# Kernel optimization log

Hardware: AMD Instinct MI355X
Metric: run time of the kernel (lower is better)

## Reference

```python
import jax, jax.numpy as jnp
import numpy as np

M, N, K = 1024, 11008, 4096


def _unpack_i2u(Bp):
    """Unpack 2-bit unsigned weights per decode_i2u_to_i8s interleave.

    Bp: [N, K//4] int8 storage. Within each group of 4 bytes (16 elements),
    output element at position 4*i + j = (byte_j >> (2*i)) & 3.
    Returns [N, K] int8 with values in {0,1,2,3}.
    """
    Bu = jax.lax.bitcast_convert_type(Bp, jnp.uint8)  # [N, K//4]
    n, kc = Bu.shape
    Bg = Bu.reshape(n, kc // 4, 1, 4)                 # [N, G, 1, j]
    shifts = (jnp.arange(4, dtype=jnp.uint8) * jnp.uint8(2)).reshape(1, 1, 4, 1)
    vals = (Bg >> shifts) & jnp.uint8(3)              # [N, G, i, j]
    return vals.reshape(n, kc * 4).astype(jnp.int8)   # [N, K]


def setup_inputs() -> dict:
    key = jax.random.key(0)
    k1, k2 = jax.random.split(key)
    A = jax.random.randint(k1, (M, K), -128, 128, dtype=jnp.int8)
    B = jax.random.randint(k2, (N, K // 4), -128, 128, dtype=jnp.int8)
    return {"A": A, "B": B}


def reference(A, B):
    W = _unpack_i2u(B)  # [N, K] int8
    C = jax.lax.dot_general(
        A, W,
        dimension_numbers=(((1,), (1,)), ((), ())),
        preferred_element_type=jnp.int32,
    )  # [M, N] int32
    return C
```

## Files before the change

### kernel.cpp

```cpp
#include <hip/hip_runtime.h>
#include <stdint.h>


#define MM 1024
#define NN 11008
#define KK 4096
#define MTILES 8
#define NTILES 86
#define NBLOCKS (16 * NTILES)
#define STRIDE_A ((size_t)MTILES * 8192)
#define STRIDE_B ((size_t)NTILES * 2048)

using i32x4  = __attribute__((ext_vector_type(4))) int;
using i32x16 = __attribute__((ext_vector_type(16))) int;

__device__ __forceinline__ int pack4(i32x4 v) {
    return (int)(((uint32_t)v[0] & 0xFFu) | (((uint32_t)v[1] & 0xFFu) << 8)
               | (((uint32_t)v[2] & 0xFFu) << 16) | (((uint32_t)v[3] & 0xFFu) << 24));
}

__global__ __launch_bounds__(256) void prep_AB(const int* __restrict__ Asrc,
                                               const int* __restrict__ Bsrc,
                                               uint8_t* __restrict__ A2,
                                               uint8_t* __restrict__ B3) {
    if (blockIdx.x < 1024) {
        const int g = blockIdx.x * 256 + threadIdx.x;
        const int kstep = g >> 12;
        const int rem   = g & 4095;
        const int mtile = rem >> 9;
        const int c     = rem & 511;
        const int row32 = (c >> 7) & 3, kk2 = (c >> 6) & 1;
        const int lane  = c & 63;
        const int row   = mtile * 128 + row32 * 32 + (lane & 31);
        const int kbyte = kstep * 64 + kk2 * 32 + (lane >> 5) * 16;
        const i32x4* s4 = (const i32x4*)(Asrc + (size_t)row * KK + kbyte);
        i32x4 o;
#pragma unroll
        for (int q = 0; q < 4; ++q) o[q] = pack4(s4[q]);
        *(i32x4*)(A2 + (size_t)g * 16) = o;
    } else {
        const int t = (blockIdx.x - 1024) * 256 + threadIdx.x;
        const int n = t >> 6, kstep = t & 63;
        const int ntile = n >> 7, hf = (n >> 6) & 1, ni = (n >> 5) & 1, l31 = n & 31;
        const i32x4* s4 = (const i32x4*)(Bsrc + (size_t)n * (KK / 4) + kstep * 16);
        int w[4];
#pragma unroll
        for (int j = 0; j < 4; ++j) w[j] = pack4(s4[j]);
        uint8_t* base = B3 + ((size_t)kstep * NTILES + ntile) * 2048 + hf * 1024;
        *(int2*)(base + l31 * 16 + ni * 8)        = make_int2(w[0], w[2]);
        *(int2*)(base + (l31 + 32) * 16 + ni * 8) = make_int2(w[1], w[3]);
    }
}

#define GLOAD_LDS16(g, l) __builtin_amdgcn_global_load_lds(                    \
        (const __attribute__((address_space(1))) uint32_t*)(g),                \
        (__attribute__((address_space(3))) uint32_t*)(l), 16, 0, 0)

#define MFMA_I8 __builtin_amdgcn_mfma_i32_32x32x32_i8

#define STAGE(T) do {                                                          \
    const uint8_t* at_ = gA + (size_t)((T) + 3) * STRIDE_A;                    \
    uint8_t* ls_ = &As[wid][((T) + 3) & 3][0];                                 \
    GLOAD_LDS16(at_,        ls_);                                              \
    GLOAD_LDS16(at_ + 1024, ls_ + 1024);                                       \
    GLOAD_LDS16(at_ + 2048, ls_ + 2048);                                       \
    GLOAD_LDS16(at_ + 3072, ls_ + 3072);                                       \
} while (0)

#define BLOAD(BI, T) do {                                                      \
    c0[BI] = *(const i32x4*)(gB + (size_t)(T) * STRIDE_B);                     \
    c1[BI] = *(const i32x4*)(gB + (size_t)(T) * STRIDE_B + 1024);              \
} while (0)

#define COMP(T, BI) do {                                                       \
    const uint8_t* ab_ = &As[wid][(T) & 3][0];                                 \
    i32x4 a00 = *(const i32x4*)(ab_ + lane * 16);                              \
    i32x4 a01 = *(const i32x4*)(ab_ + 1024 + lane * 16);                       \
    i32x4 a10 = *(const i32x4*)(ab_ + 2048 + lane * 16);                       \
    i32x4 a11 = *(const i32x4*)(ab_ + 3072 + lane * 16);                       \
    _Pragma("unroll")                                                          \
    for (int kk2_ = 0; kk2_ < 2; ++kk2_) {                                     \
        const uint32_t q0_ = (uint32_t)c0[BI][kk2_];                           \
        const uint32_t q1_ = (uint32_t)c0[BI][2 + kk2_];                       \
        const uint32_t q2_ = (uint32_t)c1[BI][kk2_];                           \
        const uint32_t q3_ = (uint32_t)c1[BI][2 + kk2_];                       \
        i32x4 b0_, b1_, b2_, b3_;                                              \
        _Pragma("unroll")                                                      \
        for (int i_ = 0; i_ < 4; ++i_) {                                       \
            b0_[i_] = (int)((q0_ >> (2 * i_)) & 0x03030303u);                  \
            b1_[i_] = (int)((q1_ >> (2 * i_)) & 0x03030303u);                  \
            b2_[i_] = (int)((q2_ >> (2 * i_)) & 0x03030303u);                  \
            b3_[i_] = (int)((q3_ >> (2 * i_)) & 0x03030303u);                  \
        }                                                                      \
        const i32x4 am0_ = kk2_ ? a01 : a00;                                   \
        const i32x4 am1_ = kk2_ ? a11 : a10;                                   \
        __builtin_amdgcn_s_setprio(1);                                         \
        acc[0][0] = MFMA_I8(am0_, b0_, acc[0][0], 0, 0, 0);                    \
        acc[0][1] = MFMA_I8(am0_, b1_, acc[0][1], 0, 0, 0);                    \
        acc[0][2] = MFMA_I8(am0_, b2_, acc[0][2], 0, 0, 0);                    \
        acc[0][3] = MFMA_I8(am0_, b3_, acc[0][3], 0, 0, 0);                    \
        acc[1][0] = MFMA_I8(am1_, b0_, acc[1][0], 0, 0, 0);                    \
        acc[1][1] = MFMA_I8(am1_, b1_, acc[1][1], 0, 0, 0);                    \
        acc[1][2] = MFMA_I8(am1_, b2_, acc[1][2], 0, 0, 0);                    \
        acc[1][3] = MFMA_I8(am1_, b3_, acc[1][3], 0, 0, 0);                    \
        __builtin_amdgcn_s_setprio(0);                                         \
    }                                                                          \
} while (0)

#define ITER(T, BCUR, BNXT, NW, DOSTAGE, DOB) do {                             \
    if (DOSTAGE) STAGE(T);                                                     \
    if (DOB)     BLOAD(BNXT, (T) + 2);                                         \
    asm volatile("s_waitcnt vmcnt(" #NW ")" ::: "memory");                     \
    __builtin_amdgcn_sched_barrier(0);                                         \
    COMP(T, BCUR);                                                             \
} while (0)

__global__ __launch_bounds__(128, 2) void bitnet_gemm(const uint8_t* __restrict__ A2,
                                                      const uint8_t* __restrict__ B3,
                                                      int* __restrict__ C) {
    const int tid  = threadIdx.x;
    const int lane = tid & 63, wid = tid >> 6;
    const int l31  = lane & 31, h = lane >> 5;

    const int bid = blockIdx.x;
    const int l   = (bid & 7) * (NBLOCKS / 8) + (bid >> 3);
    const int wm  = l & 15;
    const int wn  = l >> 4;

    __shared__ __align__(16) uint8_t As[2][4][4096];

    const uint8_t* gA = A2 + (size_t)(wid * 32) * STRIDE_A + wm * 4096 + lane * 16;
    const uint8_t* gB = B3 + (size_t)(wid * 32) * STRIDE_B + (size_t)wn * 2048 + lane * 16;

    i32x16 acc[2][4] = {};
    i32x4 c0[3], c1[3];

    STAGE(-3); STAGE(-2); STAGE(-1);
    BLOAD(0, 0); BLOAD(1, 1);

    ITER(0, 0, 2, 8, 1, 1);
    ITER(1, 1, 0, 8, 1, 1);
#pragma unroll 1
    for (int t = 2; t < 29; t += 3) {
        ITER(t,     2, 1, 12, 1, 1);
        ITER(t + 1, 0, 2, 12, 1, 1);
        ITER(t + 2, 1, 0, 12, 1, 1);
    }
    ITER(29, 2, 1, 8, 0, 1);
    ITER(30, 0, 0, 2, 0, 0);
    ITER(31, 1, 0, 0, 0, 0);

    __syncthreads();
    i32x4* red = (i32x4*)&As[0][0][0];
    if (wid == 1) {
#pragma unroll
        for (int mi = 0; mi < 2; ++mi)
#pragma unroll
            for (int nc = 0; nc < 4; ++nc) {
                const i32x16 v = acc[mi][nc];
#pragma unroll
                for (int q = 0; q < 4; ++q) {
                    i32x4 s;
                    s[0] = v[q * 4 + 0]; s[1] = v[q * 4 + 1];
                    s[2] = v[q * 4 + 2]; s[3] = v[q * 4 + 3];
                    red[((mi * 4 + nc) * 4 + q) * 64 + lane] = s;
                }
            }
    }
    __syncthreads();
    if (wid == 0) {
        const int brow = wm * 64, bcol = wn * 128;
#pragma unroll
        for (int mi = 0; mi < 2; ++mi)
#pragma unroll
            for (int nc = 0; nc < 4; ++nc) {
                i32x16 v = acc[mi][nc];
#pragma unroll
                for (int q = 0; q < 4; ++q) {
                    const i32x4 r = red[((mi * 4 + nc) * 4 + q) * 64 + lane];
                    v[q * 4 + 0] += r[0]; v[q * 4 + 1] += r[1];
                    v[q * 4 + 2] += r[2]; v[q * 4 + 3] += r[3];
                }
                const int colg = bcol + nc * 32 + l31;
#pragma unroll
                for (int r = 0; r < 16; ++r) {
                    const int rowin = (r & 3) + 8 * (r >> 2) + 4 * h;
                    const int rowg  = brow + mi * 32 + rowin;
                    C[(size_t)rowg * NN + colg] = v[r];
                }
            }
    }
}

extern "C" void kernel_launch(void* const* d_in, const int* in_sizes, int n_in,
                              void* d_out, int out_size, void* d_ws, size_t ws_size,
                              hipStream_t stream) {
    const int* A32 = (const int*)d_in[0];
    const int* B32 = (const int*)d_in[1];
    int* C = (int*)d_out;

    uint8_t* A2 = (uint8_t*)d_ws;
    uint8_t* B3 = A2 + (size_t)MM * KK;

    prep_AB<<<dim3(1024 + 2752), dim3(256), 0, stream>>>(A32, B32, A2, B3);
    bitnet_gemm<<<dim3(NBLOCKS), dim3(128), 0, stream>>>(A2, B3, C);
}
```

Baseline: 78.32 us.

## Split the N tile across waves instead of split-K, dropping the LDS reduction

The two waves in a block used to split K and each hold the full 64x128 accumulator tile, which forced a reduction through LDS at the end. Now each wave covers a 64x64 half of the N tile over the whole K range, so accumulators halve and the reduction and its barriers disappear. With the smaller register footprint, the launch bounds rise to 3 blocks per EU. The cost is that both waves now stage the same A tile into separate LDS buffers, doubling A load traffic. The pipeline also runs twice as many K iterations, each with half the MFMA work.

```diff
diff --git a/kernel.cpp b/kernel.cpp
--- a/kernel.cpp
+++ b/kernel.cpp
@@ -67,10 +67,7 @@
     GLOAD_LDS16(at_ + 3072, ls_ + 3072);                                       \
 } while (0)
 
-#define BLOAD(BI, T) do {                                                      \
-    c0[BI] = *(const i32x4*)(gB + (size_t)(T) * STRIDE_B);                     \
-    c1[BI] = *(const i32x4*)(gB + (size_t)(T) * STRIDE_B + 1024);              \
-} while (0)
+#define BLOAD(BI, T) bbuf[BI] = *(const i32x4*)(gB + (size_t)(T) * STRIDE_B)
 
 #define COMP(T, BI) do {                                                       \
     const uint8_t* ab_ = &As[wid][(T) & 3][0];                                 \
@@ -80,29 +77,21 @@
     i32x4 a11 = *(const i32x4*)(ab_ + 3072 + lane * 16);                       \
     _Pragma("unroll")                                                          \
     for (int kk2_ = 0; kk2_ < 2; ++kk2_) {                                     \
-        const uint32_t q0_ = (uint32_t)c0[BI][kk2_];                           \
-        const uint32_t q1_ = (uint32_t)c0[BI][2 + kk2_];                       \
-        const uint32_t q2_ = (uint32_t)c1[BI][kk2_];                           \
-        const uint32_t q3_ = (uint32_t)c1[BI][2 + kk2_];                       \
-        i32x4 b0_, b1_, b2_, b3_;                                              \
+        const uint32_t q0_ = (uint32_t)bbuf[BI][kk2_];                         \
+        const uint32_t q1_ = (uint32_t)bbuf[BI][2 + kk2_];                     \
+        i32x4 b0_, b1_;                                                        \
         _Pragma("unroll")                                                      \
         for (int i_ = 0; i_ < 4; ++i_) {                                       \
             b0_[i_] = (int)((q0_ >> (2 * i_)) & 0x03030303u);                  \
             b1_[i_] = (int)((q1_ >> (2 * i_)) & 0x03030303u);                  \
-            b2_[i_] = (int)((q2_ >> (2 * i_)) & 0x03030303u);                  \
-            b3_[i_] = (int)((q3_ >> (2 * i_)) & 0x03030303u);                  \
         }                                                                      \
         const i32x4 am0_ = kk2_ ? a01 : a00;                                   \
         const i32x4 am1_ = kk2_ ? a11 : a10;                                   \
         __builtin_amdgcn_s_setprio(1);                                         \
         acc[0][0] = MFMA_I8(am0_, b0_, acc[0][0], 0, 0, 0);                    \
         acc[0][1] = MFMA_I8(am0_, b1_, acc[0][1], 0, 0, 0);                    \
-        acc[0][2] = MFMA_I8(am0_, b2_, acc[0][2], 0, 0, 0);                    \
-        acc[0][3] = MFMA_I8(am0_, b3_, acc[0][3], 0, 0, 0);                    \
         acc[1][0] = MFMA_I8(am1_, b0_, acc[1][0], 0, 0, 0);                    \
         acc[1][1] = MFMA_I8(am1_, b1_, acc[1][1], 0, 0, 0);                    \
-        acc[1][2] = MFMA_I8(am1_, b2_, acc[1][2], 0, 0, 0);                    \
-        acc[1][3] = MFMA_I8(am1_, b3_, acc[1][3], 0, 0, 0);                    \
         __builtin_amdgcn_s_setprio(0);                                         \
     }                                                                          \
 } while (0)
@@ -115,7 +104,7 @@
     COMP(T, BCUR);                                                             \
 } while (0)
 
-__global__ __launch_bounds__(128, 2) void bitnet_gemm(const uint8_t* __restrict__ A2,
+__global__ __launch_bounds__(128, 3) void bitnet_gemm(const uint8_t* __restrict__ A2,
                                                       const uint8_t* __restrict__ B3,
                                                       int* __restrict__ C) {
     const int tid  = threadIdx.x;
@@ -125,71 +114,46 @@
     const int bid = blockIdx.x;
     const int l   = (bid & 7) * (NBLOCKS / 8) + (bid >> 3);
     const int wm  = l & 15;
-    const int wn  = l >> 4;
+    const int bn  = l >> 4;
 
     __shared__ __align__(16) uint8_t As[2][4][4096];
 
-    const uint8_t* gA = A2 + (size_t)(wid * 32) * STRIDE_A + wm * 4096 + lane * 16;
-    const uint8_t* gB = B3 + (size_t)(wid * 32) * STRIDE_B + (size_t)wn * 2048 + lane * 16;
+    const uint8_t* gA = A2 + (size_t)wm * 4096 + lane * 16;
+    const uint8_t* gB = B3 + (size_t)bn * 2048 + wid * 1024 + lane * 16;
 
-    i32x16 acc[2][4] = {};
-    i32x4 c0[3], c1[3];
+    i32x16 acc[2][2] = {};
+    i32x4 bbuf[3];
 
     STAGE(-3); STAGE(-2); STAGE(-1);
     BLOAD(0, 0); BLOAD(1, 1);
 
-    ITER(0, 0, 2, 8, 1, 1);
-    ITER(1, 1, 0, 8, 1, 1);
+    ITER(0, 0, 2, 6,  1, 1);
+    ITER(1, 1, 0, 10, 1, 1);
 #pragma unroll 1
-    for (int t = 2; t < 29; t += 3) {
-        ITER(t,     2, 1, 12, 1, 1);
-        ITER(t + 1, 0, 2, 12, 1, 1);
-        ITER(t + 2, 1, 0, 12, 1, 1);
+    for (int t = 2; t < 59; t += 3) {
+        ITER(t,     2, 1, 10, 1, 1);
+        ITER(t + 1, 0, 2, 10, 1, 1);
+        ITER(t + 2, 1, 0, 10, 1, 1);
     }
-    ITER(29, 2, 1, 8, 0, 1);
-    ITER(30, 0, 0, 2, 0, 0);
-    ITER(31, 1, 0, 0, 0, 0);
+    ITER(59, 2, 1, 10, 1, 1);
+    ITER(60, 0, 2, 10, 1, 1);
+    ITER(61, 1, 0, 6,  0, 1);
+    ITER(62, 2, 1, 1,  0, 0);
+    ITER(63, 0, 2, 0,  0, 0);
 
-    __syncthreads();
-    i32x4* red = (i32x4*)&As[0][0][0];
-    if (wid == 1) {
+    const int brow = wm * 64, bcol = bn * 128 + wid * 64;
 #pragma unroll
-        for (int mi = 0; mi < 2; ++mi)
+    for (int mi = 0; mi < 2; ++mi)
 #pragma unroll
-            for (int nc = 0; nc < 4; ++nc) {
-                const i32x16 v = acc[mi][nc];
+        for (int nc = 0; nc < 2; ++nc) {
+            const int colg = bcol + nc * 32 + l31;
 #pragma unroll
-                for (int q = 0; q < 4; ++q) {
-                    i32x4 s;
-                    s[0] = v[q * 4 + 0]; s[1] = v[q * 4 + 1];
-                    s[2] = v[q * 4 + 2]; s[3] = v[q * 4 + 3];
-                    red[((mi * 4 + nc) * 4 + q) * 64 + lane] = s;
-                }
+            for (int r = 0; r < 16; ++r) {
+                const int rowin = (r & 3) + 8 * (r >> 2) + 4 * h;
+                const int rowg  = brow + mi * 32 + rowin;
+                C[(size_t)rowg * NN + colg] = acc[mi][nc][r];
             }
-    }
-    __syncthreads();
-    if (wid == 0) {
-        const int brow = wm * 64, bcol = wn * 128;
-#pragma unroll
-        for (int mi = 0; mi < 2; ++mi)
-#pragma unroll
-            for (int nc = 0; nc < 4; ++nc) {
-                i32x16 v = acc[mi][nc];
-#pragma unroll
-                for (int q = 0; q < 4; ++q) {
-                    const i32x4 r = red[((mi * 4 + nc) * 4 + q) * 64 + lane];
-                    v[q * 4 + 0] += r[0]; v[q * 4 + 1] += r[1];
-                    v[q * 4 + 2] += r[2]; v[q * 4 + 3] += r[3];
-                }
-                const int colg = bcol + nc * 32 + l31;
-#pragma unroll
-                for (int r = 0; r < 16; ++r) {
-                    const int rowin = (r & 3) + 8 * (r >> 2) + 4 * h;
-                    const int rowg  = brow + mi * 32 + rowin;
-                    C[(size_t)rowg * NN + colg] = v[r];
-                }
-            }
-    }
+        }
 }
 
 extern "C" void kernel_launch(void* const* d_in, const int* in_sizes, int n_in,
```

Result: slower. 82.08 us (+4.8%).
